# Kernel tuning notes

Hardware: AMD Instinct MI355X
Metric: run time of the kernel (lower is better)

Reference implementation:

```python
import jax, jax.numpy as jnp
import numpy as np

NUM_GROUPS = 8
GROUP_SIZE = 512
FEATURE_DIM = NUM_GROUPS * GROUP_SIZE
MIN_BITS, MAX_BITS, TARGET_BITS = 2.0, 4.0 * 2, 4.0  # min=2, max=8, target=4
BIT_LEVELS = jnp.array([2.0, 4.0, 8.0], dtype=jnp.float32)
LN_EPS = 1e-5


def setup_inputs() -> dict:
    key = jax.random.key(0)
    ks = jax.random.split(key, 10)
    B, T = 16, 2048
    H = NUM_GROUPS * 2  # hidden of bit predictor
    inv8 = 1.0 / np.sqrt(NUM_GROUPS)
    invH = 1.0 / np.sqrt(H)
    return {
        "importance_scores": jax.random.normal(ks[0], (B, T, FEATURE_DIM), jnp.float32),
        "u": jax.random.uniform(ks[1], (B, NUM_GROUPS), jnp.float32),
        "W1": jax.random.uniform(ks[2], (NUM_GROUPS, H), jnp.float32, -inv8, inv8),
        "b1": jax.random.uniform(ks[3], (H,), jnp.float32, -inv8, inv8),
        "ln_g": jnp.ones((H,), jnp.float32),
        "ln_b": jnp.zeros((H,), jnp.float32),
        "W2": jax.random.uniform(ks[4], (H, NUM_GROUPS), jnp.float32, -invH, invH),
        "b2": jax.random.uniform(ks[5], (NUM_GROUPS,), jnp.float32, -invH, invH),
        "bit_embeddings": jax.random.normal(ks[6], (3, GROUP_SIZE), jnp.float32),
    }


def reference(importance_scores, u, W1, b1, ln_g, ln_b, W2, b2, bit_embeddings):
    B = importance_scores.shape[0]
    # [B,T,D] -> [B,D] -> group means [B,G]
    imp = importance_scores.mean(axis=1)
    group_imp = imp.reshape(B, NUM_GROUPS, GROUP_SIZE).mean(axis=-1)

    # tiny MLP bit predictor: Linear -> GELU -> LayerNorm -> Linear
    h = group_imp @ W1 + b1
    h = jax.nn.gelu(h, approximate=False)
    mu = h.mean(axis=-1, keepdims=True)
    var = ((h - mu) ** 2).mean(axis=-1, keepdims=True)
    h = (h - mu) * jax.lax.rsqrt(var + LN_EPS) * ln_g + ln_b
    logits = h @ W2 + b2

    # training-mode Gumbel perturbation (temperature = 1.0)
    gumbel = -jnp.log(-jnp.log(u + 1e-8) + 1e-8)
    bit_probs = jax.nn.softmax(logits + gumbel, axis=-1)

    # constrained continuous allocation
    alloc = MIN_BITS + bit_probs * (MAX_BITS - MIN_BITS)
    budget = TARGET_BITS * NUM_GROUPS
    alloc = alloc * (budget / alloc.sum(axis=-1, keepdims=True))
    alloc = jnp.clip(alloc, MIN_BITS, MAX_BITS)

    # discretize to nearest bit level with straight-through gradient
    dist = jnp.abs(alloc[..., None] - BIT_LEVELS)  # [B,G,3]
    idx = jnp.argmin(dist, axis=-1)
    hard = BIT_LEVELS[idx]
    discrete_bits = hard + alloc - jax.lax.stop_gradient(alloc)  # value == hard

    # per-group soft codebook mix: softmax(exp(-|b - level|)) @ embeddings
    bit_w = jax.nn.softmax(jnp.exp(-jnp.abs(discrete_bits[..., None] - BIT_LEVELS)), axis=-1)
    embeddings = jnp.einsum("bgl,ld->bgd", bit_w, bit_embeddings)

    group_indices = jnp.broadcast_to(
        (jnp.arange(FEATURE_DIM) // GROUP_SIZE)[None, :], (B, FEATURE_DIM)
    )
    bitrate_loss = (discrete_bits.mean() - TARGET_BITS) ** 2
    diversity_bonus = -(bit_probs * jnp.log(bit_probs + 1e-8)).sum(axis=-1).mean()
    return (discrete_bits, group_indices, embeddings, bitrate_loss, diversity_bonus, bit_probs)
```

## Files before the change

### kernel.cpp

```cpp
#include <hip/hip_runtime.h>
#include <math.h>

#define B_DIM 16
#define T_DIM 2048
#define D_DIM 4096
#define G_DIM 8
#define GS    512
#define H_DIM 16
#define CHUNKS 128
#define NPARTIAL (B_DIM * G_DIM * CHUNKS)

#define OUT_DBITS   0
#define OUT_GIDX    128
#define OUT_EMB     65664
#define OUT_BLOSS   131200
#define OUT_DIV     131201
#define OUT_BPROBS  131202

typedef float f32x4 __attribute__((ext_vector_type(4)));

__global__ __launch_bounds__(256) void k_reduce(const float* __restrict__ scores,
                                                double* __restrict__ partials) {
    const int bid   = blockIdx.x;
    const int b     = bid >> 7;
    const int chunk = bid & 127;
    const int tid   = threadIdx.x;

    const f32x4* base = reinterpret_cast<const f32x4*>(
        scores + (size_t)b * T_DIM * D_DIM + (size_t)chunk * 16 * D_DIM);

    double a0 = 0.0, a1 = 0.0, a2 = 0.0, a3 = 0.0;
    #pragma unroll 4
    for (int r = 0; r < 16; ++r) {
        const f32x4* row = base + (size_t)r * (D_DIM / 4);
        const f32x4 v0 = __builtin_nontemporal_load(row + tid);
        const f32x4 v1 = __builtin_nontemporal_load(row + tid + 256);
        const f32x4 v2 = __builtin_nontemporal_load(row + tid + 512);
        const f32x4 v3 = __builtin_nontemporal_load(row + tid + 768);
        a0 += (double)v0.x + (double)v0.y + (double)v0.z + (double)v0.w;
        a1 += (double)v1.x + (double)v1.y + (double)v1.z + (double)v1.w;
        a2 += (double)v2.x + (double)v2.y + (double)v2.z + (double)v2.w;
        a3 += (double)v3.x + (double)v3.y + (double)v3.z + (double)v3.w;
    }

    const int lane = tid & 63;
    const int wave = tid >> 6;
    __shared__ double wsum[4][4];
    double acc[4] = {a0, a1, a2, a3};
    #pragma unroll
    for (int p = 0; p < 4; ++p) {
        double v = acc[p];
        #pragma unroll
        for (int off = 32; off > 0; off >>= 1) v += __shfl_down(v, off, 64);
        if (lane == 0) wsum[wave][p] = v;
    }
    __syncthreads();

    if (tid < G_DIM) {
        const int p  = tid >> 1;
        const int w0 = (tid & 1) * 2;
        partials[(size_t)(b * G_DIM + tid) * CHUNKS + chunk] = wsum[w0][p] + wsum[w0 + 1][p];
    }
}

__device__ __forceinline__ void run_mlp(const float* __restrict__ gi8, int b,
                                        const float* __restrict__ u,
                                        const float* __restrict__ W1,
                                        const float* __restrict__ b1,
                                        const float* __restrict__ ln_g,
                                        const float* __restrict__ ln_b,
                                        const float* __restrict__ W2,
                                        const float* __restrict__ b2,
                                        float* __restrict__ p,
                                        float* __restrict__ hard,
                                        float (*bw)[3],
                                        float* entb_out, float* bs_out) {
    float h[H_DIM];
    #pragma unroll
    for (int i = 0; i < H_DIM; ++i) {
        float a = b1[i];
        #pragma unroll
        for (int g = 0; g < G_DIM; ++g) a += gi8[g] * W1[g * H_DIM + i];
        h[i] = 0.5f * a * (1.0f + erff(a * 0.70710678118654752440f));
    }
    float mu = 0.f;
    #pragma unroll
    for (int i = 0; i < H_DIM; ++i) mu += h[i];
    mu *= (1.0f / (float)H_DIM);
    float var = 0.f;
    #pragma unroll
    for (int i = 0; i < H_DIM; ++i) { float d = h[i] - mu; var += d * d; }
    var *= (1.0f / (float)H_DIM);
    const float inv = rsqrtf(var + 1e-5f);
    #pragma unroll
    for (int i = 0; i < H_DIM; ++i) h[i] = (h[i] - mu) * inv * ln_g[i] + ln_b[i];

    float z[G_DIM];
    #pragma unroll
    for (int j = 0; j < G_DIM; ++j) {
        float a = b2[j];
        #pragma unroll
        for (int i = 0; i < H_DIM; ++i) a += h[i] * W2[i * G_DIM + j];
        const float uu = u[b * G_DIM + j];
        z[j] = a + (-logf(-logf(uu + 1e-8f) + 1e-8f));
    }
    float m = z[0];
    #pragma unroll
    for (int j = 1; j < G_DIM; ++j) m = fmaxf(m, z[j]);
    float ssum = 0.f;
    #pragma unroll
    for (int j = 0; j < G_DIM; ++j) { p[j] = expf(z[j] - m); ssum += p[j]; }
    const float rs = 1.0f / ssum;

    float alloc[G_DIM]; float asum = 0.f;
    #pragma unroll
    for (int j = 0; j < G_DIM; ++j) {
        p[j] *= rs;
        alloc[j] = 2.0f + p[j] * 6.0f;
        asum += alloc[j];
    }
    const float scale = 32.0f / asum;

    float entb = 0.f, bs = 0.f;
    #pragma unroll
    for (int j = 0; j < G_DIM; ++j) {
        float a = alloc[j] * scale;
        a = fminf(fmaxf(a, 2.0f), 8.0f);
        const float hd = (a <= 3.0f) ? 2.0f : ((a <= 6.0f) ? 4.0f : 8.0f);
        hard[j] = hd;
        entb += p[j] * logf(p[j] + 1e-8f);
        bs += hd;
        const float x0 = expf(-fabsf(hd - 2.0f));
        const float x1 = expf(-fabsf(hd - 4.0f));
        const float x2 = expf(-fabsf(hd - 8.0f));
        const float mm = fmaxf(x0, fmaxf(x1, x2));
        const float e0 = expf(x0 - mm), e1 = expf(x1 - mm), e2 = expf(x2 - mm);
        const float ir = 1.0f / (e0 + e1 + e2);
        bw[j][0] = e0 * ir;
        bw[j][1] = e1 * ir;
        bw[j][2] = e2 * ir;
    }
    *entb_out = entb;
    *bs_out = bs;
}

__global__ __launch_bounds__(256) void k_tail(const double* __restrict__ partials,
                                              const float* __restrict__ u,
                                              const float* __restrict__ W1,
                                              const float* __restrict__ b1,
                                              const float* __restrict__ ln_g,
                                              const float* __restrict__ ln_b,
                                              const float* __restrict__ W2,
                                              const float* __restrict__ b2,
                                              const float* __restrict__ emb,
                                              float* __restrict__ out) {
    const int blk = blockIdx.x;
    const int b   = blk >> 2;
    const int q   = blk & 3;
    const int tid = threadIdx.x;

    __shared__ float s_gi[B_DIM * G_DIM];
    __shared__ float s_w[G_DIM][3];
    __shared__ float s_ent[B_DIM], s_bs[B_DIM];

    if (blk == 0) {
        if (tid < 128) {
            double s = 0.0;
            #pragma unroll 8
            for (int c = 0; c < CHUNKS; ++c) s += partials[(size_t)tid * CHUNKS + c];
            s_gi[tid] = (float)(s * (1.0 / ((double)T_DIM * (double)GS)));
        }
        __syncthreads();
        if (tid < B_DIM) {
            float p[G_DIM], hard[G_DIM], bw[G_DIM][3], entb, bs;
            run_mlp(&s_gi[tid * G_DIM], tid, u, W1, b1, ln_g, ln_b, W2, b2,
                    p, hard, bw, &entb, &bs);
            #pragma unroll
            for (int j = 0; j < G_DIM; ++j) {
                out[OUT_DBITS  + tid * G_DIM + j] = hard[j];
                out[OUT_BPROBS + tid * G_DIM + j] = p[j];
            }
            s_ent[tid] = entb;
            s_bs[tid]  = bs;
            if (tid == 0) {
                #pragma unroll
                for (int j = 0; j < G_DIM; ++j) {
                    s_w[j][0] = bw[j][0]; s_w[j][1] = bw[j][1]; s_w[j][2] = bw[j][2];
                }
            }
        }
        __syncthreads();
        if (tid == 0) {
            float tb = 0.f, te = 0.f;
            #pragma unroll
            for (int bb = 0; bb < B_DIM; ++bb) { tb += s_bs[bb]; te += s_ent[bb]; }
            const float mb = tb * (1.0f / (float)(B_DIM * G_DIM));
            out[OUT_BLOSS] = (mb - 4.0f) * (mb - 4.0f);
            out[OUT_DIV]   = -te * (1.0f / (float)B_DIM);
        }
    } else {
        const double* pb = partials + (size_t)b * G_DIM * CHUNKS;
        double v = 0.0;
        #pragma unroll
        for (int k = 0; k < 4; ++k) v += pb[tid * 4 + k];
        #pragma unroll
        for (int off = 16; off > 0; off >>= 1) v += __shfl_down(v, off, 32);
        if ((tid & 31) == 0)
            s_gi[tid >> 5] = (float)(v * (1.0 / ((double)T_DIM * (double)GS)));
        __syncthreads();
        if (tid == 0) {
            float p[G_DIM], hard[G_DIM], bw[G_DIM][3], entb, bs;
            run_mlp(&s_gi[0], b, u, W1, b1, ln_g, ln_b, W2, b2,
                    p, hard, bw, &entb, &bs);
            #pragma unroll
            for (int j = 0; j < G_DIM; ++j) {
                s_w[j][0] = bw[j][0]; s_w[j][1] = bw[j][1]; s_w[j][2] = bw[j][2];
            }
        }
    }
    __syncthreads();

    const int l  = blk * 256 + tid;
    const int g  = q * 2 + (tid >> 7);
    const int j4 = tid & 127;

    const float4* e4 = reinterpret_cast<const float4*>(emb);
    const float4 e0 = e4[0 * 128 + j4];
    const float4 e1 = e4[1 * 128 + j4];
    const float4 e2 = e4[2 * 128 + j4];
    const float w0 = s_w[g][0], w1 = s_w[g][1], w2 = s_w[g][2];

    float4 r;
    r.x = w0 * e0.x + w1 * e1.x + w2 * e2.x;
    r.y = w0 * e0.y + w1 * e1.y + w2 * e2.y;
    r.z = w0 * e0.z + w1 * e1.z + w2 * e2.z;
    r.w = w0 * e0.w + w1 * e1.w + w2 * e2.w;

    float4* o4 = reinterpret_cast<float4*>(out);
    o4[(OUT_EMB / 4) + l] = r;

    const float gv = (float)g;
    o4[(OUT_GIDX / 4) + l] = make_float4(gv, gv, gv, gv);
}

extern "C" void kernel_launch(void* const* d_in, const int* in_sizes, int n_in,
                              void* d_out, int out_size, void* d_ws, size_t ws_size,
                              hipStream_t stream) {
    const float* scores = (const float*)d_in[0];
    const float* u      = (const float*)d_in[1];
    const float* W1     = (const float*)d_in[2];
    const float* b1     = (const float*)d_in[3];
    const float* ln_g   = (const float*)d_in[4];
    const float* ln_b   = (const float*)d_in[5];
    const float* W2     = (const float*)d_in[6];
    const float* b2     = (const float*)d_in[7];
    const float* emb    = (const float*)d_in[8];
    float* out = (float*)d_out;

    double* partials = (double*)d_ws;

    k_reduce<<<B_DIM * CHUNKS, 256, 0, stream>>>(scores, partials);
    k_tail<<<64, 256, 0, stream>>>(partials, u, W1, b1, ln_g, ln_b, W2, b2, emb, out);
}
```

Baseline: 94.90 us.

## Fuse reduction and tail into one kernel using last-block atomic counters

Merges the streaming reduction and the MLP/embedding tail into a single kernel. The last block to finish each batch, found through an atomic counter, runs the MLP and writes that batch's embeddings, and a second global counter elects the block that computes the scalar losses. This removes the second kernel launch and its dependency gap, at the cost of a memset launch to reset the counters and serialized tail work in the final blocks.

```diff
diff --git a/kernel.cpp b/kernel.cpp
--- a/kernel.cpp
+++ b/kernel.cpp
@@ -17,53 +17,16 @@
 #define OUT_DIV     131201
 #define OUT_BPROBS  131202
 
+#define WS_PARTIALS 0
+#define WS_ENT      131072
+#define WS_BS       131136
+#define WS_BCTR     131200
+#define WS_GCTR     131264
+#define WS_CTR_BYTES 68
+
 typedef float f32x4 __attribute__((ext_vector_type(4)));
 
-__global__ __launch_bounds__(256) void k_reduce(const float* __restrict__ scores,
-                                                double* __restrict__ partials) {
-    const int bid   = blockIdx.x;
-    const int b     = bid >> 7;
-    const int chunk = bid & 127;
-    const int tid   = threadIdx.x;
-
-    const f32x4* base = reinterpret_cast<const f32x4*>(
-        scores + (size_t)b * T_DIM * D_DIM + (size_t)chunk * 16 * D_DIM);
-
-    double a0 = 0.0, a1 = 0.0, a2 = 0.0, a3 = 0.0;
-    #pragma unroll 4
-    for (int r = 0; r < 16; ++r) {
-        const f32x4* row = base + (size_t)r * (D_DIM / 4);
-        const f32x4 v0 = __builtin_nontemporal_load(row + tid);
-        const f32x4 v1 = __builtin_nontemporal_load(row + tid + 256);
-        const f32x4 v2 = __builtin_nontemporal_load(row + tid + 512);
-        const f32x4 v3 = __builtin_nontemporal_load(row + tid + 768);
-        a0 += (double)v0.x + (double)v0.y + (double)v0.z + (double)v0.w;
-        a1 += (double)v1.x + (double)v1.y + (double)v1.z + (double)v1.w;
-        a2 += (double)v2.x + (double)v2.y + (double)v2.z + (double)v2.w;
-        a3 += (double)v3.x + (double)v3.y + (double)v3.z + (double)v3.w;
-    }
-
-    const int lane = tid & 63;
-    const int wave = tid >> 6;
-    __shared__ double wsum[4][4];
-    double acc[4] = {a0, a1, a2, a3};
-    #pragma unroll
-    for (int p = 0; p < 4; ++p) {
-        double v = acc[p];
-        #pragma unroll
-        for (int off = 32; off > 0; off >>= 1) v += __shfl_down(v, off, 64);
-        if (lane == 0) wsum[wave][p] = v;
-    }
-    __syncthreads();
-
-    if (tid < G_DIM) {
-        const int p  = tid >> 1;
-        const int w0 = (tid & 1) * 2;
-        partials[(size_t)(b * G_DIM + tid) * CHUNKS + chunk] = wsum[w0][p] + wsum[w0 + 1][p];
-    }
-}
-
-__device__ __forceinline__ void run_mlp(const float* __restrict__ gi8, int b,
+__device__ __forceinline__ void run_mlp(const float* gi8, int b,
                                         const float* __restrict__ u,
                                         const float* __restrict__ W1,
                                         const float* __restrict__ b1,
@@ -71,8 +34,8 @@
                                         const float* __restrict__ ln_b,
                                         const float* __restrict__ W2,
                                         const float* __restrict__ b2,
-                                        float* __restrict__ p,
-                                        float* __restrict__ hard,
+                                        float* p,
+                                        float* hard,
                                         float (*bw)[3],
                                         float* entb_out, float* bs_out) {
     float h[H_DIM];
@@ -112,19 +75,19 @@
     for (int j = 0; j < G_DIM; ++j) { p[j] = expf(z[j] - m); ssum += p[j]; }
     const float rs = 1.0f / ssum;
 
-    float alloc[G_DIM]; float asum = 0.f;
+    float asum = 0.f;
     #pragma unroll
     for (int j = 0; j < G_DIM; ++j) {
         p[j] *= rs;
-        alloc[j] = 2.0f + p[j] * 6.0f;
-        asum += alloc[j];
+        z[j] = 2.0f + p[j] * 6.0f;
+        asum += z[j];
     }
     const float scale = 32.0f / asum;
 
     float entb = 0.f, bs = 0.f;
     #pragma unroll
     for (int j = 0; j < G_DIM; ++j) {
-        float a = alloc[j] * scale;
+        float a = z[j] * scale;
         a = fminf(fmaxf(a, 2.0f), 8.0f);
         const float hd = (a <= 3.0f) ? 2.0f : ((a <= 6.0f) ? 4.0f : 8.0f);
         hard[j] = hd;
@@ -144,7 +107,7 @@
     *bs_out = bs;
 }
 
-__global__ __launch_bounds__(256) void k_tail(const double* __restrict__ partials,
+__global__ __launch_bounds__(256) void k_main(const float* __restrict__ scores,
                                               const float* __restrict__ u,
                                               const float* __restrict__ W1,
                                               const float* __restrict__ b1,
@@ -153,94 +116,130 @@
                                               const float* __restrict__ W2,
                                               const float* __restrict__ b2,
                                               const float* __restrict__ emb,
-                                              float* __restrict__ out) {
-    const int blk = blockIdx.x;
-    const int b   = blk >> 2;
-    const int q   = blk & 3;
-    const int tid = threadIdx.x;
-
-    __shared__ float s_gi[B_DIM * G_DIM];
-    __shared__ float s_w[G_DIM][3];
-    __shared__ float s_ent[B_DIM], s_bs[B_DIM];
-
-    if (blk == 0) {
-        if (tid < 128) {
-            double s = 0.0;
-            #pragma unroll 8
-            for (int c = 0; c < CHUNKS; ++c) s += partials[(size_t)tid * CHUNKS + c];
-            s_gi[tid] = (float)(s * (1.0 / ((double)T_DIM * (double)GS)));
-        }
-        __syncthreads();
-        if (tid < B_DIM) {
-            float p[G_DIM], hard[G_DIM], bw[G_DIM][3], entb, bs;
-            run_mlp(&s_gi[tid * G_DIM], tid, u, W1, b1, ln_g, ln_b, W2, b2,
-                    p, hard, bw, &entb, &bs);
-            #pragma unroll
-            for (int j = 0; j < G_DIM; ++j) {
-                out[OUT_DBITS  + tid * G_DIM + j] = hard[j];
-                out[OUT_BPROBS + tid * G_DIM + j] = p[j];
-            }
-            s_ent[tid] = entb;
-            s_bs[tid]  = bs;
-            if (tid == 0) {
-                #pragma unroll
-                for (int j = 0; j < G_DIM; ++j) {
-                    s_w[j][0] = bw[j][0]; s_w[j][1] = bw[j][1]; s_w[j][2] = bw[j][2];
-                }
-            }
-        }
-        __syncthreads();
-        if (tid == 0) {
-            float tb = 0.f, te = 0.f;
-            #pragma unroll
-            for (int bb = 0; bb < B_DIM; ++bb) { tb += s_bs[bb]; te += s_ent[bb]; }
-            const float mb = tb * (1.0f / (float)(B_DIM * G_DIM));
-            out[OUT_BLOSS] = (mb - 4.0f) * (mb - 4.0f);
-            out[OUT_DIV]   = -te * (1.0f / (float)B_DIM);
-        }
-    } else {
-        const double* pb = partials + (size_t)b * G_DIM * CHUNKS;
-        double v = 0.0;
-        #pragma unroll
-        for (int k = 0; k < 4; ++k) v += pb[tid * 4 + k];
-        #pragma unroll
-        for (int off = 16; off > 0; off >>= 1) v += __shfl_down(v, off, 32);
-        if ((tid & 31) == 0)
-            s_gi[tid >> 5] = (float)(v * (1.0 / ((double)T_DIM * (double)GS)));
-        __syncthreads();
-        if (tid == 0) {
-            float p[G_DIM], hard[G_DIM], bw[G_DIM][3], entb, bs;
-            run_mlp(&s_gi[0], b, u, W1, b1, ln_g, ln_b, W2, b2,
-                    p, hard, bw, &entb, &bs);
-            #pragma unroll
-            for (int j = 0; j < G_DIM; ++j) {
-                s_w[j][0] = bw[j][0]; s_w[j][1] = bw[j][1]; s_w[j][2] = bw[j][2];
-            }
-        }
-    }
-    __syncthreads();
-
-    const int l  = blk * 256 + tid;
-    const int g  = q * 2 + (tid >> 7);
-    const int j4 = tid & 127;
+                                              float* __restrict__ out,
+                                              void* __restrict__ ws) {
+    double* partials = (double*)((char*)ws + WS_PARTIALS);
+    float*  ws_ent   = (float*)((char*)ws + WS_ENT);
+    float*  ws_bs    = (float*)((char*)ws + WS_BS);
+    unsigned* bctr   = (unsigned*)((char*)ws + WS_BCTR);
+    unsigned* gctr   = (unsigned*)((char*)ws + WS_GCTR);
+
+    const int bid   = blockIdx.x;
+    const int b     = bid >> 7;
+    const int chunk = bid & 127;
+    const int tid   = threadIdx.x;
+
+    float4* o4 = reinterpret_cast<float4*>(out);
+
+    if (bid < 64) {
+        const int l   = bid * 256 + tid;
+        const int g   = (l >> 7) & 7;
+        const float gv = (float)g;
+        o4[(OUT_GIDX / 4) + l] = make_float4(gv, gv, gv, gv);
+    }
+
+    const f32x4* base = reinterpret_cast<const f32x4*>(
+        scores + (size_t)b * T_DIM * D_DIM + (size_t)chunk * 16 * D_DIM);
+
+    double a0 = 0.0, a1 = 0.0, a2 = 0.0, a3 = 0.0;
+    #pragma unroll 4
+    for (int r = 0; r < 16; ++r) {
+        const f32x4* row = base + (size_t)r * (D_DIM / 4);
+        const f32x4 v0 = __builtin_nontemporal_load(row + tid);
+        const f32x4 v1 = __builtin_nontemporal_load(row + tid + 256);
+        const f32x4 v2 = __builtin_nontemporal_load(row + tid + 512);
+        const f32x4 v3 = __builtin_nontemporal_load(row + tid + 768);
+        a0 += (double)v0.x + (double)v0.y + (double)v0.z + (double)v0.w;
+        a1 += (double)v1.x + (double)v1.y + (double)v1.z + (double)v1.w;
+        a2 += (double)v2.x + (double)v2.y + (double)v2.z + (double)v2.w;
+        a3 += (double)v3.x + (double)v3.y + (double)v3.z + (double)v3.w;
+    }
+
+    const int lane = tid & 63;
+    const int wave = tid >> 6;
+    __shared__ double wsum[4][4];
+    __shared__ int s_fin, s_fin2;
+    if (tid == 0) { s_fin = 0; s_fin2 = 0; }
+    double acc[4] = {a0, a1, a2, a3};
+    #pragma unroll
+    for (int p = 0; p < 4; ++p) {
+        double v = acc[p];
+        #pragma unroll
+        for (int off = 32; off > 0; off >>= 1) v += __shfl_down(v, off, 64);
+        if (lane == 0) wsum[wave][p] = v;
+    }
+    __syncthreads();
+
+    if (tid < G_DIM) {
+        const int p  = tid >> 1;
+        const int w0 = (tid & 1) * 2;
+        partials[(size_t)(b * G_DIM + tid) * CHUNKS + chunk] = wsum[w0][p] + wsum[w0 + 1][p];
+        __threadfence();
+        if (atomicAdd(&bctr[b], 1u) == (unsigned)(CHUNKS * G_DIM - 1)) s_fin = 1;
+    }
+    __syncthreads();
+    if (!s_fin) return;
+
+    __threadfence();
+
+    __shared__ float s_gi[G_DIM];
+    __shared__ float s_p[G_DIM], s_hard[G_DIM], s_w[G_DIM][3];
+    __shared__ float s_entb, s_bsb;
+
+    const double* pb = partials + (size_t)b * G_DIM * CHUNKS;
+    double v = 0.0;
+    #pragma unroll
+    for (int k = 0; k < 4; ++k) v += pb[tid * 4 + k];
+    #pragma unroll
+    for (int off = 16; off > 0; off >>= 1) v += __shfl_down(v, off, 32);
+    if ((tid & 31) == 0)
+        s_gi[tid >> 5] = (float)(v * (1.0 / ((double)T_DIM * (double)GS)));
+    __syncthreads();
+
+    if (tid == 0)
+        run_mlp(s_gi, b, u, W1, b1, ln_g, ln_b, W2, b2,
+                s_p, s_hard, s_w, &s_entb, &s_bsb);
+    __syncthreads();
+
+    if (tid < G_DIM) {
+        out[OUT_DBITS  + b * G_DIM + tid] = s_hard[tid];
+        out[OUT_BPROBS + b * G_DIM + tid] = s_p[tid];
+    }
+    if (tid == 0) {
+        ws_ent[b] = s_entb;
+        ws_bs[b]  = s_bsb;
+        __threadfence();
+        if (atomicAdd(gctr, 1u) == (unsigned)(B_DIM - 1)) s_fin2 = 1;
+    }
 
     const float4* e4 = reinterpret_cast<const float4*>(emb);
-    const float4 e0 = e4[0 * 128 + j4];
-    const float4 e1 = e4[1 * 128 + j4];
-    const float4 e2 = e4[2 * 128 + j4];
-    const float w0 = s_w[g][0], w1 = s_w[g][1], w2 = s_w[g][2];
-
-    float4 r;
-    r.x = w0 * e0.x + w1 * e1.x + w2 * e2.x;
-    r.y = w0 * e0.y + w1 * e1.y + w2 * e2.y;
-    r.z = w0 * e0.z + w1 * e1.z + w2 * e2.z;
-    r.w = w0 * e0.w + w1 * e1.w + w2 * e2.w;
-
-    float4* o4 = reinterpret_cast<float4*>(out);
-    o4[(OUT_EMB / 4) + l] = r;
-
-    const float gv = (float)g;
-    o4[(OUT_GIDX / 4) + l] = make_float4(gv, gv, gv, gv);
+    #pragma unroll
+    for (int i = 0; i < 4; ++i) {
+        const int k  = tid + 256 * i;
+        const int g  = k >> 7;
+        const int j4 = k & 127;
+        const float4 e0 = e4[0 * 128 + j4];
+        const float4 e1 = e4[1 * 128 + j4];
+        const float4 e2 = e4[2 * 128 + j4];
+        const float w0 = s_w[g][0], w1 = s_w[g][1], w2 = s_w[g][2];
+        float4 r;
+        r.x = w0 * e0.x + w1 * e1.x + w2 * e2.x;
+        r.y = w0 * e0.y + w1 * e1.y + w2 * e2.y;
+        r.z = w0 * e0.z + w1 * e1.z + w2 * e2.z;
+        r.w = w0 * e0.w + w1 * e1.w + w2 * e2.w;
+        o4[(OUT_EMB / 4) + b * 1024 + k] = r;
+    }
+
+    __syncthreads();
+    if (s_fin2 && tid == 0) {
+        __threadfence();
+        float tb = 0.f, te = 0.f;
+        #pragma unroll
+        for (int bb = 0; bb < B_DIM; ++bb) { tb += ws_bs[bb]; te += ws_ent[bb]; }
+        const float mb = tb * (1.0f / (float)(B_DIM * G_DIM));
+        out[OUT_BLOSS] = (mb - 4.0f) * (mb - 4.0f);
+        out[OUT_DIV]   = -te * (1.0f / (float)B_DIM);
+    }
 }
 
 extern "C" void kernel_launch(void* const* d_in, const int* in_sizes, int n_in,
@@ -257,8 +256,8 @@
     const float* emb    = (const float*)d_in[8];
     float* out = (float*)d_out;
 
-    double* partials = (double*)d_ws;
-
-    k_reduce<<<B_DIM * CHUNKS, 256, 0, stream>>>(scores, partials);
-    k_tail<<<64, 256, 0, stream>>>(partials, u, W1, b1, ln_g, ln_b, W2, b2, emb, out);
+    hipMemsetAsync((char*)d_ws + WS_BCTR, 0, WS_CTR_BYTES, stream);
+
+    k_main<<<B_DIM * CHUNKS, 256, 0, stream>>>(scores, u, W1, b1, ln_g, ln_b,
+                                               W2, b2, emb, out, d_ws);
 }
```

Result: slower. 223.9 us (+136.0%).
